# Kernel tuning notes

Measured on AMD Instinct MI355X. Metric: run time of the kernel, lower is better.

## Reference

```python
import jax, jax.numpy as jnp
import numpy as np

DIM = 64
WS = 8    # window_size
SS = 4    # shift_size


def _conv(x, w, pad, groups=1):
    return jax.lax.conv_general_dilated(
        x, w, (1, 1), ((pad, pad), (pad, pad)),
        dimension_numbers=('NCHW', 'OIHW', 'NCHW'),
        feature_group_count=groups)


def _window_partition(x, ws):
    # x: (B, C, H, W) -> (B*Hn*Wn, C, ws, ws), with bottom/right padding
    B, C, H, W = x.shape
    pb = (-H) % ws
    pr = (-W) % ws
    x = jnp.pad(x, ((0, 0), (0, 0), (0, pb), (0, pr)))
    Hp, Wp = H + pb, W + pr
    x = x.reshape(B, C, Hp // ws, ws, Wp // ws, ws).transpose(0, 1, 2, 4, 3, 5)
    return x.reshape(-1, C, ws, ws)


def _window_reverse(wins, ws, H, W):
    pb = (-H) % ws
    pr = (-W) % ws
    Hp, Wp = H + pb, W + pr
    B = wins.shape[0] // ((Hp // ws) * (Wp // ws))
    x = wins.reshape(B, -1, Hp // ws, Wp // ws, ws, ws).transpose(0, 1, 2, 4, 3, 5)
    x = x.reshape(B, -1, Hp, Wp)
    return x[:, :, :H, :W]


def _create_mask(H, W, ws, ss):
    # Swin-style additive mask, computed statically with numpy
    Hp = int(np.ceil(H / ws)) * ws
    Wp = int(np.ceil(W / ws)) * ws
    m = np.zeros((Hp, Wp), dtype=np.float32)
    slices = (slice(0, -ws), slice(-ws, -ss), slice(-ss, None))
    cnt = 0
    for hs in slices:
        for wsl in slices:
            m[hs, wsl] = cnt
            cnt += 1
    mw = m.reshape(Hp // ws, ws, Wp // ws, ws).transpose(0, 2, 1, 3).reshape(-1, ws * ws)
    diff = mw[:, None, :] - mw[:, :, None]
    return jnp.asarray(np.where(diff != 0, -100.0, 0.0).astype(np.float32))


def _l2norm(x):
    # matches torch F.normalize(dim=-1, eps=1e-12)
    return x / jnp.maximum(jnp.linalg.norm(x, axis=-1, keepdims=True), 1e-12)


def _win_attn(xw, w_qkv, w_dw, w_proj, ws, mask, b):
    # xw: (N, C, ws, ws) windows
    C = xw.shape[1]
    qkv = _conv(_conv(xw, w_qkv, 0), w_dw, 1, groups=3 * C)
    q, k, v = jnp.split(qkv, 3, axis=1)
    N = q.shape[0]
    hw = ws * ws
    q = _l2norm(q.reshape(N, C, hw))
    k = _l2norm(k.reshape(N, C, hw))
    v = v.reshape(N, C, hw)
    attn = jnp.einsum('nci,ncj->nij', q, k) / ws  # (N, hw, hw)
    if mask is not None:
        attn = (attn.reshape(b, -1, hw, hw) + mask[None]).reshape(-1, hw, hw)
    attn = jax.nn.softmax(attn, axis=-1)
    out = jnp.einsum('nci,nij->ncj', v, attn).reshape(N, C, ws, ws)
    return _conv(out, w_proj, 1)


def _forward(x, w_qkv0, w_dw0, w_proj0, w_qkv1, w_dw1, w_proj1):
    b, c, h, w = x.shape
    # pass 1: unshifted windows
    xw = _window_partition(x, WS)
    out = _win_attn(xw, w_qkv0, w_dw0, w_proj0, WS, None, b)
    out = _window_reverse(out, WS, h, w)
    # pass 2: shifted windows with Swin mask
    shift = jnp.roll(out, (-SS, -SS), axis=(2, 3))
    sw = _window_partition(shift, WS)
    mask = _create_mask(h, w, WS, SS)
    out = _win_attn(sw, w_qkv1, w_dw1, w_proj1, WS, mask, b)
    out = _window_reverse(out, WS, h, w)
    return jnp.roll(out, (SS, SS), axis=(2, 3))


def setup_inputs() -> dict:
    key = jax.random.key(0)
    ks = jax.random.split(key, 7)
    C = DIM
    s = 0.05
    return {
        'x': jax.random.normal(ks[0], (8, C, 256, 256), jnp.float32),
        'w_qkv0': jax.random.normal(ks[1], (3 * C, C, 1, 1), jnp.float32) * s,
        'w_dw0': jax.random.normal(ks[2], (3 * C, 1, 3, 3), jnp.float32) * s,
        'w_proj0': jax.random.normal(ks[3], (C, C, 3, 3), jnp.float32) * s,
        'w_qkv1': jax.random.normal(ks[4], (3 * C, C, 1, 1), jnp.float32) * s,
        'w_dw1': jax.random.normal(ks[5], (3 * C, 1, 3, 3), jnp.float32) * s,
        'w_proj1': jax.random.normal(ks[6], (C, C, 3, 3), jnp.float32) * s,
    }


def reference(x, w_qkv0, w_dw0, w_proj0, w_qkv1, w_dw1, w_proj1):
    return _forward(x, w_qkv0, w_dw0, w_proj0, w_qkv1, w_dw1, w_proj1)
```

## Files before the change

kernel.cpp:

```cpp
#include <hip/hip_runtime.h>


typedef __attribute__((ext_vector_type(8))) short bf8;
typedef __attribute__((ext_vector_type(4))) float f32x4;
#define MFMA(a, b, c) __builtin_amdgcn_mfma_f32_16x16x32_bf16(a, b, c, 0, 0, 0)

__device__ __forceinline__ int xkey(int p) { return ((p >> 3) ^ p) & 7; }
__device__ __forceinline__ int xswz(int p, int c) { return p * 64 + (c ^ (xkey(p) << 3)); }
__device__ __forceinline__ int pswz68(int ch, int p) {
    return ch * 68 + (p ^ (((ch >> 1) & 7) << 2));
}

__device__ __forceinline__ unsigned cvtpk(float a, float b) {
    unsigned r;
    asm("v_cvt_pk_bf16_f32 %0, %1, %2" : "=v"(r) : "v"(a), "v"(b));
    return r;
}

__device__ __forceinline__ void bsplit(float f, short& h, short& l) {
    unsigned u = __float_as_uint(f);
    unsigned hb = (u + 0x7FFFu + ((u >> 16) & 1u)) >> 16;
    float hf = __uint_as_float(hb << 16);
    float r = f - hf;
    unsigned u2 = __float_as_uint(r);
    unsigned lb = (u2 + 0x7FFFu + ((u2 >> 16) & 1u)) >> 16;
    h = (short)hb; l = (short)lb;
}
__device__ __forceinline__ void bsplit2(float a, float b, unsigned& hw, unsigned& lw) {
    hw = cvtpk(a, b);
    float ra = a - __uint_as_float(hw << 16);
    float rb = b - __uint_as_float(hw & 0xFFFF0000u);
    lw = cvtpk(ra, rb);
}

__global__ void k_fq(const float* __restrict__ wq, short* __restrict__ oh, short* __restrict__ ol) {
    int bx = blockIdx.x;
    int kk = bx / 12, tt = bx % 12;
    int tid = threadIdx.x;
    int lane = tid >> 3, j = tid & 7;
    int oc = tt * 16 + (lane & 15);
    int ic = kk * 32 + ((lane >> 4) << 3) + j;
    short h, l; bsplit(wq[oc * 64 + ic], h, l);
    oh[bx * 512 + tid] = h; ol[bx * 512 + tid] = l;
}
__global__ void k_fp(const float* __restrict__ wp, short* __restrict__ oh, short* __restrict__ ol) {
    int bx = blockIdx.x;
    int tap = bx >> 3, kk = (bx >> 2) & 1, tt = bx & 3;
    int tid = threadIdx.x;
    int lane = tid >> 3, j = tid & 7;
    int oc = tt * 16 + (lane & 15);
    int ic = kk * 32 + ((lane >> 4) << 3) + j;
    short h, l; bsplit(wp[(oc * 64 + ic) * 9 + tap], h, l);
    oh[bx * 512 + tid] = h; ol[bx * 512 + tid] = l;
}

__device__ __forceinline__ void dw_pair(const float* scr, const float* wd9,
                                        int ch0, int row, float o[2][8]) {
    #pragma unroll
    for (int chi = 0; chi < 2; ++chi) {
        int ch = ch0 + chi;
        const float* wd = wd9 + ch * 9;
        float w9[9];
        #pragma unroll
        for (int tp = 0; tp < 9; ++tp) w9[tp] = wd[tp];
        float e[3][10];
        #pragma unroll
        for (int k3 = 0; k3 < 3; ++k3) {
            int rr = row - 1 + k3;
            e[k3][0] = 0.f; e[k3][9] = 0.f;
            if ((unsigned)rr < 8u) {
                float4 a = *(const float4*)&scr[pswz68(ch, rr * 8)];
                float4 b = *(const float4*)&scr[pswz68(ch, rr * 8 + 4)];
                e[k3][1] = a.x; e[k3][2] = a.y; e[k3][3] = a.z; e[k3][4] = a.w;
                e[k3][5] = b.x; e[k3][6] = b.y; e[k3][7] = b.z; e[k3][8] = b.w;
            } else {
                #pragma unroll
                for (int q2 = 1; q2 < 9; ++q2) e[k3][q2] = 0.f;
            }
        }
        #pragma unroll
        for (int s = 0; s < 8; ++s) {
            float a = 0.f;
            #pragma unroll
            for (int k3 = 0; k3 < 3; ++k3)
                #pragma unroll
                for (int dx = 0; dx < 3; ++dx)
                    a = fmaf(w9[k3 * 3 + dx], e[k3][s + dx], a);
            o[chi][s] = a;
        }
    }
}

__device__ __forceinline__ void p2_chunk(const short* XTh, const short* XTl,
                                         const short* bqh, const short* bql,
                                         float* scr, int chunk,
                                         int mh, int nh, int col, int quad, int qo8, int lane)
{
    f32x4 acc[2][2];
    #pragma unroll
    for (int mt = 0; mt < 2; ++mt)
        #pragma unroll
        for (int nt = 0; nt < 2; ++nt) acc[mt][nt] = (f32x4){0.f, 0.f, 0.f, 0.f};
    #pragma unroll
    for (int kk = 0; kk < 2; ++kk) {
        bf8 Ah[2], Al[2];
        #pragma unroll
        for (int mt = 0; mt < 2; ++mt) {
            int row = (mh * 2 + mt) * 16 + col;
            int ad = row * 64 + ((kk * 32 + qo8) ^ (xkey(row) << 3));
            Ah[mt] = *(const bf8*)&XTh[ad];
            Al[mt] = *(const bf8*)&XTl[ad];
        }
        #pragma unroll
        for (int nt = 0; nt < 2; ++nt) {
            int tt = chunk * 4 + nh * 2 + nt;
            bf8 Bh = *(const bf8*)&bqh[((kk * 12 + tt) * 64 + lane) * 8];
            bf8 Bl = *(const bf8*)&bql[((kk * 12 + tt) * 64 + lane) * 8];
            #pragma unroll
            for (int mt = 0; mt < 2; ++mt) {
                acc[mt][nt] = MFMA(Ah[mt], Bh, acc[mt][nt]);
                acc[mt][nt] = MFMA(Ah[mt], Bl, acc[mt][nt]);
                acc[mt][nt] = MFMA(Al[mt], Bh, acc[mt][nt]);
            }
        }
    }
    #pragma unroll
    for (int nt = 0; nt < 2; ++nt) {
        int oc = (nh * 2 + nt) * 16 + col;
        #pragma unroll
        for (int mt = 0; mt < 2; ++mt) {
            int p0 = (mh * 2 + mt) * 16 + quad * 4;
            *(f32x4*)&scr[pswz68(oc, p0)] = acc[mt][nt];
        }
    }
}

__global__ __launch_bounds__(256, 3)
void k_fused(const float* __restrict__ in,
             const short* __restrict__ bqh, const short* __restrict__ bql,
             const float* __restrict__ wdw,
             const short* __restrict__ bph, const short* __restrict__ bpl,
             float* __restrict__ out, int shift, int use_mask, int roll)
{
    __shared__ __align__(16) char smem[50432];
    short* XTh = (short*)smem;
    short* XTl = (short*)(smem + 8320);
    float* scr = (float*)(smem + 16640);
    short* vbh = (short*)(smem + 16640);
    short* vbl = (short*)(smem + 24832);
    float* projo = (float*)(smem + 16640);
    short* kTh = (short*)(smem + 34048);
    short* kTl = (short*)(smem + 42240);
    short* PTh = kTh;
    short* PTl = kTl;

    const int tid = threadIdx.x, lane = tid & 63, wv = tid >> 6;
    const int col = lane & 15, quad = lane >> 4, qo8 = quad * 8;
    const int mh = wv & 1, nh = wv >> 1;
    const int cp = tid >> 3, rrow = tid & 7;
    const int n = blockIdx.x;
    const int b = n >> 10, c = (n >> 4) & 63, t = n & 15;
    const size_t base = ((size_t)(b * 64 + c)) << 16;

    #pragma unroll
    for (int k = 0; k < 16; k += 2) {
        int o0 = tid + k * 256, o1 = o0 + 256;
        int hi0 = o0 >> 11, r0 = (o0 >> 8) & 7, lo0 = (o0 >> 3) & 31, s0 = o0 & 7;
        int hi1 = o1 >> 11, r1 = (o1 >> 8) & 7, lo1 = (o1 >> 3) & 31, s1 = o1 & 7;
        float v0 = in[base + (size_t)(((t * 16 + hi0 * 8 + r0) + shift) & 255) * 256
                           + (((lo0 * 8 + s0) + shift) & 255)];
        float v1 = in[base + (size_t)(((t * 16 + hi1 * 8 + r1) + shift) & 255) * 256
                           + (((lo1 * 8 + s1) + shift) & 255)];
        unsigned hw, lw; bsplit2(v0, v1, hw, lw);
        int ad0 = xswz(r0 * 8 + s0, hi0 * 32 + lo0);
        int ad1 = xswz(r1 * 8 + s1, hi1 * 32 + lo1);
        XTh[ad0] = (short)hw; XTh[ad1] = (short)(hw >> 16);
        XTl[ad0] = (short)lw; XTl[ad1] = (short)(lw >> 16);
    }
    __syncthreads();

    p2_chunk(XTh, XTl, bqh, bql, scr, 0, mh, nh, col, quad, qo8, lane);
    __syncthreads();

    float dq[2][8], nq[2];
    dw_pair(scr, wdw, 2 * cp, rrow, dq);
    #pragma unroll
    for (int chi = 0; chi < 2; ++chi) {
        float ss = 0.f;
        #pragma unroll
        for (int s = 0; s < 8; ++s) ss = fmaf(dq[chi][s], dq[chi][s], ss);
        ss += __shfl_xor(ss, 1); ss += __shfl_xor(ss, 2); ss += __shfl_xor(ss, 4);
        nq[chi] = fmaxf(sqrtf(ss), 1e-12f);
    }
    __syncthreads();

    p2_chunk(XTh, XTl, bqh, bql, scr, 1, mh, nh, col, quad, qo8, lane);
    __syncthreads();

    {
        float dk[2][8];
        dw_pair(scr, wdw + 64 * 9, 2 * cp, rrow, dk);
        #pragma unroll
        for (int chi = 0; chi < 2; ++chi) {
            float ss = 0.f;
            #pragma unroll
            for (int s = 0; s < 8; ++s) ss = fmaf(dk[chi][s], dk[chi][s], ss);
            ss += __shfl_xor(ss, 1); ss += __shfl_xor(ss, 2); ss += __shfl_xor(ss, 4);
            float nk = fmaxf(sqrtf(ss), 1e-12f);
            float sc = 0.125f / (nq[chi] * nk);
            #pragma unroll
            for (int s = 0; s < 8; ++s) dk[chi][s] *= sc;
        }
        #pragma unroll
        for (int s0 = 0; s0 < 8; ++s0) {
            unsigned hw, lw; bsplit2(dk[0][s0], dk[1][s0], hw, lw);
            int ad = xswz(rrow * 8 + s0, 2 * cp);
            *(unsigned*)&kTh[ad] = hw; *(unsigned*)&kTl[ad] = lw;
        }
    }
    __syncthreads();

    p2_chunk(XTh, XTl, bqh, bql, scr, 2, mh, nh, col, quad, qo8, lane);
    __syncthreads();

    float dv[2][8];
    dw_pair(scr, wdw + 128 * 9, 2 * cp, rrow, dv);
    #pragma unroll
    for (int s0 = 0; s0 < 8; ++s0) {
        unsigned hw, lw; bsplit2(dq[0][s0], dq[1][s0], hw, lw);
        int ad = xswz(rrow * 8 + s0, 2 * cp);
        *(unsigned*)&XTh[ad] = hw; *(unsigned*)&XTl[ad] = lw;
    }
    if (tid < 32) {
        *(unsigned*)&XTh[4096 + 2 * tid] = 0u;
        *(unsigned*)&XTl[4096 + 2 * tid] = 0u;
    }
    __syncthreads();

    #pragma unroll
    for (int chi = 0; chi < 2; ++chi) {
        unsigned hw[4], lw[4];
        #pragma unroll
        for (int q2 = 0; q2 < 4; ++q2) bsplit2(dv[chi][2 * q2], dv[chi][2 * q2 + 1], hw[q2], lw[q2]);
        int ch = 2 * cp + chi;
        int ad = ch * 64 + ((rrow ^ xkey(ch)) << 3);
        *(uint4*)&vbh[ad] = (uint4){hw[0], hw[1], hw[2], hw[3]};
        *(uint4*)&vbl[ad] = (uint4){lw[0], lw[1], lw[2], lw[3]};
    }

    f32x4 at[4];
    #pragma unroll
    for (int nt = 0; nt < 4; ++nt) at[nt] = (f32x4){0.f, 0.f, 0.f, 0.f};
    {
        bf8 Ah[2], Al[2];
        #pragma unroll
        for (int kk = 0; kk < 2; ++kk) {
            int row = wv * 16 + col;
            int ad = row * 64 + ((kk * 32 + qo8) ^ (xkey(row) << 3));
            Ah[kk] = *(const bf8*)&XTh[ad];
            Al[kk] = *(const bf8*)&XTl[ad];
        }
        #pragma unroll
        for (int kk = 0; kk < 2; ++kk)
            #pragma unroll
            for (int nt = 0; nt < 4; ++nt) {
                int rowB = nt * 16 + col;
                int ad = rowB * 64 + ((kk * 32 + qo8) ^ (xkey(rowB) << 3));
                bf8 Bh = *(const bf8*)&kTh[ad];
                bf8 Bl = *(const bf8*)&kTl[ad];
                at[nt] = MFMA(Ah[kk], Bh, at[nt]);
                at[nt] = MFMA(Ah[kk], Bl, at[nt]);
                at[nt] = MFMA(Al[kk], Bh, at[nt]);
            }
    }
    if (use_mask) {
        const int widx = n & 1023;
        const int hn_m = widx >> 5, wn_m = widx & 31;
        #pragma unroll
        for (int nt = 0; nt < 4; ++nt) {
            int j = nt * 16 + col;
            int rj = ((hn_m == 31) ? (((j >> 3) < 4) ? 1 : 2) : 0) * 3
                   + ((wn_m == 31) ? (((j & 7) < 4) ? 1 : 2) : 0);
            #pragma unroll
            for (int rg = 0; rg < 4; ++rg) {
                int i = wv * 16 + quad * 4 + rg;
                int ri = ((hn_m == 31) ? (((i >> 3) < 4) ? 1 : 2) : 0) * 3
                       + ((wn_m == 31) ? (((i & 7) < 4) ? 1 : 2) : 0);
                if (ri != rj) at[nt][rg] = at[nt][rg] - 100.f;
            }
        }
    }
    float Pv[4][4];
    #pragma unroll
    for (int rg = 0; rg < 4; ++rg) {
        float m = fmaxf(fmaxf(at[0][rg], at[1][rg]), fmaxf(at[2][rg], at[3][rg]));
        m = fmaxf(m, __shfl_xor(m, 1)); m = fmaxf(m, __shfl_xor(m, 2));
        m = fmaxf(m, __shfl_xor(m, 4)); m = fmaxf(m, __shfl_xor(m, 8));
        float e0 = __expf(at[0][rg] - m), e1 = __expf(at[1][rg] - m);
        float e2 = __expf(at[2][rg] - m), e3 = __expf(at[3][rg] - m);
        float s = e0 + e1 + e2 + e3;
        s += __shfl_xor(s, 1); s += __shfl_xor(s, 2);
        s += __shfl_xor(s, 4); s += __shfl_xor(s, 8);
        float is = 1.0f / s;
        Pv[0][rg] = e0 * is; Pv[1][rg] = e1 * is; Pv[2][rg] = e2 * is; Pv[3][rg] = e3 * is;
    }
    __syncthreads();

    #pragma unroll
    for (int nt = 0; nt < 4; ++nt) {
        int j = nt * 16 + col;
        #pragma unroll
        for (int rp = 0; rp < 2; ++rp) {
            unsigned hw, lw; bsplit2(Pv[nt][2 * rp], Pv[nt][2 * rp + 1], hw, lw);
            int i0 = wv * 16 + quad * 4 + 2 * rp;
            int ad = j * 64 + (i0 ^ (xkey(j) << 3));
            *(unsigned*)&PTh[ad] = hw; *(unsigned*)&PTl[ad] = lw;
        }
    }
    __syncthreads();

    {
        f32x4 av[2][2];
        #pragma unroll
        for (int mt = 0; mt < 2; ++mt)
            #pragma unroll
            for (int nt = 0; nt < 2; ++nt) av[mt][nt] = (f32x4){0.f, 0.f, 0.f, 0.f};
        #pragma unroll
        for (int kk = 0; kk < 2; ++kk) {
            bf8 Ah[2], Al[2], Bh[2], Bl[2];
            #pragma unroll
            for (int mt = 0; mt < 2; ++mt) {
                int row = (mh * 2 + mt) * 16 + col;
                int ad = row * 64 + ((kk * 32 + qo8) ^ (xkey(row) << 3));
                Ah[mt] = *(const bf8*)&vbh[ad];
                Al[mt] = *(const bf8*)&vbl[ad];
            }
            #pragma unroll
            for (int nt = 0; nt < 2; ++nt) {
                int rowB = (nh * 2 + nt) * 16 + col;
                int ad = rowB * 64 + ((kk * 32 + qo8) ^ (xkey(rowB) << 3));
                Bh[nt] = *(const bf8*)&PTh[ad];
                Bl[nt] = *(const bf8*)&PTl[ad];
            }
            #pragma unroll
            for (int mt = 0; mt < 2; ++mt)
                #pragma unroll
                for (int nt = 0; nt < 2; ++nt) {
                    av[mt][nt] = MFMA(Ah[mt], Bh[nt], av[mt][nt]);
                    av[mt][nt] = MFMA(Ah[mt], Bl[nt], av[mt][nt]);
                    av[mt][nt] = MFMA(Al[mt], Bh[nt], av[mt][nt]);
                }
        }
        #pragma unroll
        for (int nt = 0; nt < 2; ++nt) {
            int j = (nh * 2 + nt) * 16 + col;
            #pragma unroll
            for (int mt = 0; mt < 2; ++mt) {
                int c0 = (mh * 2 + mt) * 16 + quad * 4;
                #pragma unroll
                for (int rp = 0; rp < 2; ++rp) {
                    unsigned hw, lw; bsplit2(av[mt][nt][2 * rp], av[mt][nt][2 * rp + 1], hw, lw);
                    int ad = j * 64 + ((c0 + 2 * rp) ^ (xkey(j) << 3));
                    *(unsigned*)&XTh[ad] = hw;
                    *(unsigned*)&XTl[ad] = lw;
                }
            }
        }
    }
    __syncthreads();

    {
        f32x4 ap[2][2];
        #pragma unroll
        for (int mt = 0; mt < 2; ++mt)
            #pragma unroll
            for (int nt = 0; nt < 2; ++nt) ap[mt][nt] = (f32x4){0.f, 0.f, 0.f, 0.f};
        const int smc = col & 7;
        #pragma unroll 1
        for (int tap = 0; tap < 9; ++tap) {
            int dy = (tap >= 6) ? 1 : ((tap >= 3) ? 0 : -1);
            int dx = tap - (dy + 1) * 3 - 1;
            int ra[2];
            #pragma unroll
            for (int mt = 0; mt < 2; ++mt) {
                int rr = (mh * 2 + mt) * 2 + (col >> 3) + dy;
                int ss = smc + dx;
                bool ok = ((unsigned)rr < 8u) && ((unsigned)ss < 8u);
                ra[mt] = ok ? (rr * 8 + ss) : 64;
            }
            #pragma unroll
            for (int kk = 0; kk < 2; ++kk) {
                bf8 Bh[2], Bl[2], Ah[2], Al[2];
                #pragma unroll
                for (int nt = 0; nt < 2; ++nt) {
                    int bi = (((tap * 2 + kk) * 4 + (nh * 2 + nt)) * 64 + lane) * 8;
                    Bh[nt] = *(const bf8*)&bph[bi];
                    Bl[nt] = *(const bf8*)&bpl[bi];
                }
                #pragma unroll
                for (int mt = 0; mt < 2; ++mt) {
                    int ad = ra[mt] * 64 + ((kk * 32 + qo8) ^ (xkey(ra[mt]) << 3));
                    Ah[mt] = *(const bf8*)&XTh[ad];
                    Al[mt] = *(const bf8*)&XTl[ad];
                }
                #pragma unroll
                for (int mt = 0; mt < 2; ++mt)
                    #pragma unroll
                    for (int nt = 0; nt < 2; ++nt) {
                        ap[mt][nt] = MFMA(Ah[mt], Bh[nt], ap[mt][nt]);
                        ap[mt][nt] = MFMA(Ah[mt], Bl[nt], ap[mt][nt]);
                        ap[mt][nt] = MFMA(Al[mt], Bh[nt], ap[mt][nt]);
                    }
            }
        }
        #pragma unroll
        for (int nt = 0; nt < 2; ++nt) {
            int oc = (nh * 2 + nt) * 16 + col;
            #pragma unroll
            for (int mt = 0; mt < 2; ++mt) {
                int p0 = (mh * 2 + mt) * 16 + quad * 4;
                *(f32x4*)&projo[pswz68(oc, p0)] = ap[mt][nt];
            }
        }
    }
    __syncthreads();

    #pragma unroll
    for (int k = 0; k < 16; ++k) {
        int o = tid + k * 256;
        int hi = o >> 11, r = (o >> 8) & 7, lo = (o >> 3) & 31, s = o & 7;
        int c2 = hi * 32 + lo;
        float v = projo[pswz68(c2, r * 8 + s)];
        int h2 = t * 16 + hi * 8 + r, w2 = lo * 8 + s;
        out[base + (size_t)((h2 + roll) & 255) * 256 + ((w2 + roll) & 255)] = v;
    }
}

extern "C" void kernel_launch(void* const* d_in, const int* in_sizes, int n_in,
                              void* d_out, int out_size, void* d_ws, size_t ws_size,
                              hipStream_t stream)
{
    const float* x      = (const float*)d_in[0];
    const float* wqkv0  = (const float*)d_in[1];
    const float* wdw0   = (const float*)d_in[2];
    const float* wproj0 = (const float*)d_in[3];
    const float* wqkv1  = (const float*)d_in[4];
    const float* wdw1   = (const float*)d_in[5];
    const float* wproj1 = (const float*)d_in[6];
    float* out = (float*)d_out;

    float* tmp = (float*)d_ws;
    short* fb  = (short*)(tmp + 33554432);
    short* bq0h = fb;
    short* bq0l = fb + 12288;
    short* bq1h = fb + 24576;
    short* bq1l = fb + 36864;
    short* bp0h = fb + 49152;
    short* bp0l = fb + 86016;
    short* bp1h = fb + 122880;
    short* bp1l = fb + 159744;

    hipLaunchKernelGGL(k_fq, dim3(24), dim3(512), 0, stream, wqkv0, bq0h, bq0l);
    hipLaunchKernelGGL(k_fq, dim3(24), dim3(512), 0, stream, wqkv1, bq1h, bq1l);
    hipLaunchKernelGGL(k_fp, dim3(72), dim3(512), 0, stream, wproj0, bp0h, bp0l);
    hipLaunchKernelGGL(k_fp, dim3(72), dim3(512), 0, stream, wproj1, bp1h, bp1l);

    hipLaunchKernelGGL(k_fused, dim3(8192), dim3(256), 0, stream,
                       x, bq0h, bq0l, wdw0, bp0h, bp0l, tmp, 0, 0, 0);
    hipLaunchKernelGGL(k_fused, dim3(8192), dim3(256), 0, stream,
                       tmp, bq1h, bq1l, wdw1, bp1h, bp1l, out, 4, 1, 4);
}
```

Baseline: 635.6 us.

## Shrink shared memory to fit four blocks per CU by chunking QKV and PV stages

Cuts the fused window-attention kernel's LDS footprint from about 50KB to 40KB and raises the launch bound from 3 to 4 blocks per CU. The QKV projection is now computed in six 32-channel chunks instead of three 64-channel ones, and each thread handles one channel instead of two in the depthwise conv. The P·V stage is split into two halves that reuse a smaller P buffer. Buffers are aliased more aggressively, and the zero-padding row for the projection conv moves to a separate location. The aim is higher occupancy, paid for with more __syncthreads barriers and smaller MFMA tiles per wave.

```diff
diff --git a/kernel.cpp b/kernel.cpp
--- a/kernel.cpp
+++ b/kernel.cpp
@@ -7,8 +7,11 @@
 
 __device__ __forceinline__ int xkey(int p) { return ((p >> 3) ^ p) & 7; }
 __device__ __forceinline__ int xswz(int p, int c) { return p * 64 + (c ^ (xkey(p) << 3)); }
-__device__ __forceinline__ int pswz68(int ch, int p) {
-    return ch * 68 + (p ^ (((ch >> 1) & 7) << 2));
+__device__ __forceinline__ int sswz(int ch, int p) {
+    return ch * 64 + (p ^ (((ch >> 1) & 7) << 2));
+}
+__device__ __forceinline__ int jswz(int ch, int p) {
+    return ch * 64 + (p ^ (((ch >> 1) & 7) << 3));
 }
 
 __device__ __forceinline__ unsigned cvtpk(float a, float b) {
@@ -54,53 +57,54 @@
     oh[bx * 512 + tid] = h; ol[bx * 512 + tid] = l;
 }
 
-__device__ __forceinline__ void dw_pair(const float* scr, const float* wd9,
-                                        int ch0, int row, float o[2][8]) {
-    #pragma unroll
-    for (int chi = 0; chi < 2; ++chi) {
-        int ch = ch0 + chi;
-        const float* wd = wd9 + ch * 9;
-        float w9[9];
-        #pragma unroll
-        for (int tp = 0; tp < 9; ++tp) w9[tp] = wd[tp];
-        float e[3][10];
-        #pragma unroll
-        for (int k3 = 0; k3 < 3; ++k3) {
-            int rr = row - 1 + k3;
-            e[k3][0] = 0.f; e[k3][9] = 0.f;
-            if ((unsigned)rr < 8u) {
-                float4 a = *(const float4*)&scr[pswz68(ch, rr * 8)];
-                float4 b = *(const float4*)&scr[pswz68(ch, rr * 8 + 4)];
-                e[k3][1] = a.x; e[k3][2] = a.y; e[k3][3] = a.z; e[k3][4] = a.w;
-                e[k3][5] = b.x; e[k3][6] = b.y; e[k3][7] = b.z; e[k3][8] = b.w;
-            } else {
-                #pragma unroll
-                for (int q2 = 1; q2 < 9; ++q2) e[k3][q2] = 0.f;
-            }
-        }
-        #pragma unroll
-        for (int s = 0; s < 8; ++s) {
-            float a = 0.f;
-            #pragma unroll
-            for (int k3 = 0; k3 < 3; ++k3)
-                #pragma unroll
-                for (int dx = 0; dx < 3; ++dx)
-                    a = fmaf(w9[k3 * 3 + dx], e[k3][s + dx], a);
-            o[chi][s] = a;
-        }
-    }
-}
-
-__device__ __forceinline__ void p2_chunk(const short* XTh, const short* XTl,
-                                         const short* bqh, const short* bql,
-                                         float* scr, int chunk,
-                                         int mh, int nh, int col, int quad, int qo8, int lane)
+__device__ __forceinline__ void dw_one(const float* scr, const float* wd,
+                                       int ch, int row, float o[8]) {
+    float w9[9];
+    #pragma unroll
+    for (int tp = 0; tp < 9; ++tp) w9[tp] = wd[tp];
+    float e[3][10];
+    #pragma unroll
+    for (int k3 = 0; k3 < 3; ++k3) {
+        int rr = row - 1 + k3;
+        e[k3][0] = 0.f; e[k3][9] = 0.f;
+        if ((unsigned)rr < 8u) {
+            float4 a = *(const float4*)&scr[sswz(ch, rr * 8)];
+            float4 b = *(const float4*)&scr[sswz(ch, rr * 8 + 4)];
+            e[k3][1] = a.x; e[k3][2] = a.y; e[k3][3] = a.z; e[k3][4] = a.w;
+            e[k3][5] = b.x; e[k3][6] = b.y; e[k3][7] = b.z; e[k3][8] = b.w;
+        } else {
+            #pragma unroll
+            for (int q2 = 1; q2 < 9; ++q2) e[k3][q2] = 0.f;
+        }
+    }
+    #pragma unroll
+    for (int s = 0; s < 8; ++s) {
+        float a = 0.f;
+        #pragma unroll
+        for (int k3 = 0; k3 < 3; ++k3)
+            #pragma unroll
+            for (int dx = 0; dx < 3; ++dx)
+                a = fmaf(w9[k3 * 3 + dx], e[k3][s + dx], a);
+        o[s] = a;
+    }
+}
+
+__device__ __forceinline__ float norm8(const float d[8]) {
+    float ss = 0.f;
+    #pragma unroll
+    for (int s = 0; s < 8; ++s) ss = fmaf(d[s], d[s], ss);
+    ss += __shfl_xor(ss, 1); ss += __shfl_xor(ss, 2); ss += __shfl_xor(ss, 4);
+    return fmaxf(sqrtf(ss), 1e-12f);
+}
+
+__device__ __forceinline__ void p2_chunk32(const short* XTh, const short* XTl,
+                                           const short* bqh, const short* bql,
+                                           float* scr, int chunk,
+                                           int mh, int nh, int col, int quad, int qo8, int lane)
 {
-    f32x4 acc[2][2];
-    #pragma unroll
-    for (int mt = 0; mt < 2; ++mt)
-        #pragma unroll
-        for (int nt = 0; nt < 2; ++nt) acc[mt][nt] = (f32x4){0.f, 0.f, 0.f, 0.f};
+    f32x4 acc[2];
+    #pragma unroll
+    for (int mt = 0; mt < 2; ++mt) acc[mt] = (f32x4){0.f, 0.f, 0.f, 0.f};
     #pragma unroll
     for (int kk = 0; kk < 2; ++kk) {
         bf8 Ah[2], Al[2];
@@ -111,53 +115,47 @@
             Ah[mt] = *(const bf8*)&XTh[ad];
             Al[mt] = *(const bf8*)&XTl[ad];
         }
-        #pragma unroll
-        for (int nt = 0; nt < 2; ++nt) {
-            int tt = chunk * 4 + nh * 2 + nt;
-            bf8 Bh = *(const bf8*)&bqh[((kk * 12 + tt) * 64 + lane) * 8];
-            bf8 Bl = *(const bf8*)&bql[((kk * 12 + tt) * 64 + lane) * 8];
-            #pragma unroll
-            for (int mt = 0; mt < 2; ++mt) {
-                acc[mt][nt] = MFMA(Ah[mt], Bh, acc[mt][nt]);
-                acc[mt][nt] = MFMA(Ah[mt], Bl, acc[mt][nt]);
-                acc[mt][nt] = MFMA(Al[mt], Bh, acc[mt][nt]);
-            }
-        }
-    }
-    #pragma unroll
-    for (int nt = 0; nt < 2; ++nt) {
-        int oc = (nh * 2 + nt) * 16 + col;
+        int tt = chunk * 2 + nh;
+        bf8 Bh = *(const bf8*)&bqh[((kk * 12 + tt) * 64 + lane) * 8];
+        bf8 Bl = *(const bf8*)&bql[((kk * 12 + tt) * 64 + lane) * 8];
         #pragma unroll
         for (int mt = 0; mt < 2; ++mt) {
-            int p0 = (mh * 2 + mt) * 16 + quad * 4;
-            *(f32x4*)&scr[pswz68(oc, p0)] = acc[mt][nt];
-        }
-    }
-}
-
-__global__ __launch_bounds__(256, 3)
+            acc[mt] = MFMA(Ah[mt], Bh, acc[mt]);
+            acc[mt] = MFMA(Ah[mt], Bl, acc[mt]);
+            acc[mt] = MFMA(Al[mt], Bh, acc[mt]);
+        }
+    }
+    #pragma unroll
+    for (int mt = 0; mt < 2; ++mt) {
+        int ocl = nh * 16 + col;
+        int p0 = (mh * 2 + mt) * 16 + quad * 4;
+        *(f32x4*)&scr[sswz(ocl, p0)] = acc[mt];
+    }
+}
+
+__global__ __launch_bounds__(256, 4)
 void k_fused(const float* __restrict__ in,
              const short* __restrict__ bqh, const short* __restrict__ bql,
              const float* __restrict__ wdw,
              const short* __restrict__ bph, const short* __restrict__ bpl,
              float* __restrict__ out, int shift, int use_mask, int roll)
 {
-    __shared__ __align__(16) char smem[50432];
+    __shared__ __align__(16) char smem[40960];
     short* XTh = (short*)smem;
-    short* XTl = (short*)(smem + 8320);
-    float* scr = (float*)(smem + 16640);
-    short* vbh = (short*)(smem + 16640);
-    short* vbl = (short*)(smem + 24832);
-    float* projo = (float*)(smem + 16640);
-    short* kTh = (short*)(smem + 34048);
-    short* kTl = (short*)(smem + 42240);
-    short* PTh = kTh;
-    short* PTl = kTl;
+    short* XTl = (short*)(smem + 8192);
+    short* kTh = (short*)(smem + 16384);
+    short* kTl = (short*)(smem + 24576);
+    short* vbh = kTh;
+    short* vbl = kTl;
+    float* scr = (float*)(smem + 32768);
+    short* PTh = (short*)(smem + 32768);
+    short* PTl = (short*)(smem + 36864);
+    float* projo = (float*)(smem + 16384);
 
     const int tid = threadIdx.x, lane = tid & 63, wv = tid >> 6;
     const int col = lane & 15, quad = lane >> 4, qo8 = quad * 8;
     const int mh = wv & 1, nh = wv >> 1;
-    const int cp = tid >> 3, rrow = tid & 7;
+    const int ch = tid >> 3, rrow = tid & 7;
     const int n = blockIdx.x;
     const int b = n >> 10, c = (n >> 4) & 63, t = n & 15;
     const size_t base = ((size_t)(b * 64 + c)) << 16;
@@ -179,74 +177,83 @@
     }
     __syncthreads();
 
-    p2_chunk(XTh, XTl, bqh, bql, scr, 0, mh, nh, col, quad, qo8, lane);
-    __syncthreads();
-
-    float dq[2][8], nq[2];
-    dw_pair(scr, wdw, 2 * cp, rrow, dq);
-    #pragma unroll
-    for (int chi = 0; chi < 2; ++chi) {
-        float ss = 0.f;
-        #pragma unroll
-        for (int s = 0; s < 8; ++s) ss = fmaf(dq[chi][s], dq[chi][s], ss);
-        ss += __shfl_xor(ss, 1); ss += __shfl_xor(ss, 2); ss += __shfl_xor(ss, 4);
-        nq[chi] = fmaxf(sqrtf(ss), 1e-12f);
-    }
-    __syncthreads();
-
-    p2_chunk(XTh, XTl, bqh, bql, scr, 1, mh, nh, col, quad, qo8, lane);
-    __syncthreads();
-
+    float dqA[8], dqB[8], dvA[8], dvB[8];
+    float nqA, nqB;
+
+    p2_chunk32(XTh, XTl, bqh, bql, scr, 0, mh, nh, col, quad, qo8, lane);
+    __syncthreads();
+    dw_one(scr, wdw + ch * 9, ch, rrow, dqA);
+    nqA = norm8(dqA);
+    __syncthreads();
+    p2_chunk32(XTh, XTl, bqh, bql, scr, 1, mh, nh, col, quad, qo8, lane);
+    __syncthreads();
+    dw_one(scr, wdw + (32 + ch) * 9, ch, rrow, dqB);
+    nqB = norm8(dqB);
+    __syncthreads();
+    p2_chunk32(XTh, XTl, bqh, bql, scr, 2, mh, nh, col, quad, qo8, lane);
+    __syncthreads();
     {
-        float dk[2][8];
-        dw_pair(scr, wdw + 64 * 9, 2 * cp, rrow, dk);
-        #pragma unroll
-        for (int chi = 0; chi < 2; ++chi) {
-            float ss = 0.f;
-            #pragma unroll
-            for (int s = 0; s < 8; ++s) ss = fmaf(dk[chi][s], dk[chi][s], ss);
-            ss += __shfl_xor(ss, 1); ss += __shfl_xor(ss, 2); ss += __shfl_xor(ss, 4);
-            float nk = fmaxf(sqrtf(ss), 1e-12f);
-            float sc = 0.125f / (nq[chi] * nk);
-            #pragma unroll
-            for (int s = 0; s < 8; ++s) dk[chi][s] *= sc;
-        }
-        #pragma unroll
-        for (int s0 = 0; s0 < 8; ++s0) {
-            unsigned hw, lw; bsplit2(dk[0][s0], dk[1][s0], hw, lw);
-            int ad = xswz(rrow * 8 + s0, 2 * cp);
-            *(unsigned*)&kTh[ad] = hw; *(unsigned*)&kTl[ad] = lw;
-        }
-    }
-    __syncthreads();
-
-    p2_chunk(XTh, XTl, bqh, bql, scr, 2, mh, nh, col, quad, qo8, lane);
-    __syncthreads();
-
-    float dv[2][8];
-    dw_pair(scr, wdw + 128 * 9, 2 * cp, rrow, dv);
-    #pragma unroll
-    for (int s0 = 0; s0 < 8; ++s0) {
-        unsigned hw, lw; bsplit2(dq[0][s0], dq[1][s0], hw, lw);
-        int ad = xswz(rrow * 8 + s0, 2 * cp);
-        *(unsigned*)&XTh[ad] = hw; *(unsigned*)&XTl[ad] = lw;
-    }
-    if (tid < 32) {
-        *(unsigned*)&XTh[4096 + 2 * tid] = 0u;
-        *(unsigned*)&XTl[4096 + 2 * tid] = 0u;
-    }
-    __syncthreads();
-
-    #pragma unroll
-    for (int chi = 0; chi < 2; ++chi) {
-        unsigned hw[4], lw[4];
-        #pragma unroll
-        for (int q2 = 0; q2 < 4; ++q2) bsplit2(dv[chi][2 * q2], dv[chi][2 * q2 + 1], hw[q2], lw[q2]);
-        int ch = 2 * cp + chi;
-        int ad = ch * 64 + ((rrow ^ xkey(ch)) << 3);
-        *(uint4*)&vbh[ad] = (uint4){hw[0], hw[1], hw[2], hw[3]};
-        *(uint4*)&vbl[ad] = (uint4){lw[0], lw[1], lw[2], lw[3]};
-    }
+        float dk[8];
+        dw_one(scr, wdw + (64 + ch) * 9, ch, rrow, dk);
+        float sc = 0.125f / (nqA * norm8(dk));
+        #pragma unroll
+        for (int s = 0; s < 8; ++s) dk[s] *= sc;
+        #pragma unroll
+        for (int s0 = 0; s0 < 8; s0 += 2) {
+            unsigned hw, lw; bsplit2(dk[s0], dk[s0 + 1], hw, lw);
+            int p0 = rrow * 8 + s0;
+            int a0 = xswz(p0, ch), a1 = xswz(p0 + 1, ch);
+            kTh[a0] = (short)hw; kTh[a1] = (short)(hw >> 16);
+            kTl[a0] = (short)lw; kTl[a1] = (short)(lw >> 16);
+        }
+    }
+    __syncthreads();
+    p2_chunk32(XTh, XTl, bqh, bql, scr, 3, mh, nh, col, quad, qo8, lane);
+    __syncthreads();
+    {
+        float dk[8];
+        dw_one(scr, wdw + (96 + ch) * 9, ch, rrow, dk);
+        float sc = 0.125f / (nqB * norm8(dk));
+        #pragma unroll
+        for (int s = 0; s < 8; ++s) dk[s] *= sc;
+        int cg = 32 + ch;
+        #pragma unroll
+        for (int s0 = 0; s0 < 8; s0 += 2) {
+            unsigned hw, lw; bsplit2(dk[s0], dk[s0 + 1], hw, lw);
+            int p0 = rrow * 8 + s0;
+            int a0 = xswz(p0, cg), a1 = xswz(p0 + 1, cg);
+            kTh[a0] = (short)hw; kTh[a1] = (short)(hw >> 16);
+            kTl[a0] = (short)lw; kTl[a1] = (short)(lw >> 16);
+        }
+    }
+    __syncthreads();
+    p2_chunk32(XTh, XTl, bqh, bql, scr, 4, mh, nh, col, quad, qo8, lane);
+    __syncthreads();
+    dw_one(scr, wdw + (128 + ch) * 9, ch, rrow, dvA);
+    __syncthreads();
+    p2_chunk32(XTh, XTl, bqh, bql, scr, 5, mh, nh, col, quad, qo8, lane);
+    __syncthreads();
+    dw_one(scr, wdw + (160 + ch) * 9, ch, rrow, dvB);
+    #pragma unroll
+    for (int s0 = 0; s0 < 8; s0 += 2) {
+        unsigned hw, lw; bsplit2(dqA[s0], dqA[s0 + 1], hw, lw);
+        int p0 = rrow * 8 + s0;
+        int a0 = xswz(p0, ch), a1 = xswz(p0 + 1, ch);
+        XTh[a0] = (short)hw; XTh[a1] = (short)(hw >> 16);
+        XTl[a0] = (short)lw; XTl[a1] = (short)(lw >> 16);
+    }
+    {
+        int cg = 32 + ch;
+        #pragma unroll
+        for (int s0 = 0; s0 < 8; s0 += 2) {
+            unsigned hw, lw; bsplit2(dqB[s0], dqB[s0 + 1], hw, lw);
+            int p0 = rrow * 8 + s0;
+            int a0 = xswz(p0, cg), a1 = xswz(p0 + 1, cg);
+            XTh[a0] = (short)hw; XTh[a1] = (short)(hw >> 16);
+            XTl[a0] = (short)lw; XTl[a1] = (short)(lw >> 16);
+        }
+    }
+    __syncthreads();
 
     f32x4 at[4];
     #pragma unroll
@@ -307,27 +314,53 @@
     __syncthreads();
 
     #pragma unroll
-    for (int nt = 0; nt < 4; ++nt) {
-        int j = nt * 16 + col;
+    for (int hf = 0; hf < 2; ++hf) {
+        const float* dv = hf ? dvB : dvA;
+        int cg = hf * 32 + ch;
+        unsigned hw[4], lw[4];
+        #pragma unroll
+        for (int q2 = 0; q2 < 4; ++q2) bsplit2(dv[2 * q2], dv[2 * q2 + 1], hw[q2], lw[q2]);
+        int ad = cg * 64 + ((rrow ^ xkey(cg)) << 3);
+        *(uint4*)&vbh[ad] = (uint4){hw[0], hw[1], hw[2], hw[3]};
+        *(uint4*)&vbl[ad] = (uint4){lw[0], lw[1], lw[2], lw[3]};
+    }
+    #pragma unroll
+    for (int q = 0; q < 2; ++q) {
+        int nt = q;
+        int jl = q * 16 + col;
         #pragma unroll
         for (int rp = 0; rp < 2; ++rp) {
             unsigned hw, lw; bsplit2(Pv[nt][2 * rp], Pv[nt][2 * rp + 1], hw, lw);
             int i0 = wv * 16 + quad * 4 + 2 * rp;
-            int ad = j * 64 + (i0 ^ (xkey(j) << 3));
+            int ad = jl * 64 + (i0 ^ (xkey(jl) << 3));
             *(unsigned*)&PTh[ad] = hw; *(unsigned*)&PTl[ad] = lw;
         }
     }
     __syncthreads();
 
-    {
-        f32x4 av[2][2];
-        #pragma unroll
-        for (int mt = 0; mt < 2; ++mt)
-            #pragma unroll
-            for (int nt = 0; nt < 2; ++nt) av[mt][nt] = (f32x4){0.f, 0.f, 0.f, 0.f};
+    #pragma unroll
+    for (int h = 0; h < 2; ++h) {
+        if (h == 1) {
+            #pragma unroll
+            for (int q = 0; q < 2; ++q) {
+                int nt = 2 + q;
+                int jl = q * 16 + col;
+                #pragma unroll
+                for (int rp = 0; rp < 2; ++rp) {
+                    unsigned hw, lw; bsplit2(Pv[nt][2 * rp], Pv[nt][2 * rp + 1], hw, lw);
+                    int i0 = wv * 16 + quad * 4 + 2 * rp;
+                    int ad = jl * 64 + (i0 ^ (xkey(jl) << 3));
+                    *(unsigned*)&PTh[ad] = hw; *(unsigned*)&PTl[ad] = lw;
+                }
+            }
+            __syncthreads();
+        }
+        f32x4 av[2];
+        #pragma unroll
+        for (int mt = 0; mt < 2; ++mt) av[mt] = (f32x4){0.f, 0.f, 0.f, 0.f};
         #pragma unroll
         for (int kk = 0; kk < 2; ++kk) {
-            bf8 Ah[2], Al[2], Bh[2], Bl[2];
+            bf8 Ah[2], Al[2];
             #pragma unroll
             for (int mt = 0; mt < 2; ++mt) {
                 int row = (mh * 2 + mt) * 16 + col;
@@ -335,38 +368,33 @@
                 Ah[mt] = *(const bf8*)&vbh[ad];
                 Al[mt] = *(const bf8*)&vbl[ad];
             }
-            #pragma unroll
-            for (int nt = 0; nt < 2; ++nt) {
-                int rowB = (nh * 2 + nt) * 16 + col;
-                int ad = rowB * 64 + ((kk * 32 + qo8) ^ (xkey(rowB) << 3));
-                Bh[nt] = *(const bf8*)&PTh[ad];
-                Bl[nt] = *(const bf8*)&PTl[ad];
-            }
-            #pragma unroll
-            for (int mt = 0; mt < 2; ++mt)
-                #pragma unroll
-                for (int nt = 0; nt < 2; ++nt) {
-                    av[mt][nt] = MFMA(Ah[mt], Bh[nt], av[mt][nt]);
-                    av[mt][nt] = MFMA(Ah[mt], Bl[nt], av[mt][nt]);
-                    av[mt][nt] = MFMA(Al[mt], Bh[nt], av[mt][nt]);
-                }
-        }
-        #pragma unroll
-        for (int nt = 0; nt < 2; ++nt) {
-            int j = (nh * 2 + nt) * 16 + col;
+            int jl = nh * 16 + col;
+            int bd = jl * 64 + ((kk * 32 + qo8) ^ (xkey(jl) << 3));
+            bf8 Bh = *(const bf8*)&PTh[bd];
+            bf8 Bl = *(const bf8*)&PTl[bd];
             #pragma unroll
             for (int mt = 0; mt < 2; ++mt) {
-                int c0 = (mh * 2 + mt) * 16 + quad * 4;
-                #pragma unroll
-                for (int rp = 0; rp < 2; ++rp) {
-                    unsigned hw, lw; bsplit2(av[mt][nt][2 * rp], av[mt][nt][2 * rp + 1], hw, lw);
-                    int ad = j * 64 + ((c0 + 2 * rp) ^ (xkey(j) << 3));
-                    *(unsigned*)&XTh[ad] = hw;
-                    *(unsigned*)&XTl[ad] = lw;
-                }
-            }
-        }
-    }
+                av[mt] = MFMA(Ah[mt], Bh, av[mt]);
+                av[mt] = MFMA(Ah[mt], Bl, av[mt]);
+                av[mt] = MFMA(Al[mt], Bh, av[mt]);
+            }
+        }
+        int j = (h * 2 + nh) * 16 + col;
+        #pragma unroll
+        for (int mt = 0; mt < 2; ++mt) {
+            int c0 = (mh * 2 + mt) * 16 + quad * 4;
+            #pragma unroll
+            for (int rp = 0; rp < 2; ++rp) {
+                unsigned hw, lw; bsplit2(av[mt][2 * rp], av[mt][2 * rp + 1], hw, lw);
+                int ad = j * 64 + ((c0 + 2 * rp) ^ (xkey(j) << 3));
+                *(unsigned*)&XTh[ad] = hw;
+                *(unsigned*)&XTl[ad] = lw;
+            }
+        }
+        __syncthreads();
+    }
+
+    if (tid < 32) ((unsigned*)(smem + 32768))[tid] = 0u;
     __syncthreads();
 
     {
@@ -380,13 +408,15 @@
         for (int tap = 0; tap < 9; ++tap) {
             int dy = (tap >= 6) ? 1 : ((tap >= 3) ? 0 : -1);
             int dx = tap - (dy + 1) * 3 - 1;
-            int ra[2];
+            int ra_h[2], ra_l[2];
             #pragma unroll
             for (int mt = 0; mt < 2; ++mt) {
                 int rr = (mh * 2 + mt) * 2 + (col >> 3) + dy;
                 int ss = smc + dx;
                 bool ok = ((unsigned)rr < 8u) && ((unsigned)ss < 8u);
-                ra[mt] = ok ? (rr * 8 + ss) : 64;
+                int row = rr * 8 + ss;
+                ra_h[mt] = ok ? row : 256;
+                ra_l[mt] = ok ? row : 192;
             }
             #pragma unroll
             for (int kk = 0; kk < 2; ++kk) {
@@ -399,9 +429,10 @@
                 }
                 #pragma unroll
                 for (int mt = 0; mt < 2; ++mt) {
-                    int ad = ra[mt] * 64 + ((kk * 32 + qo8) ^ (xkey(ra[mt]) << 3));
-                    Ah[mt] = *(const bf8*)&XTh[ad];
-                    Al[mt] = *(const bf8*)&XTl[ad];
+                    int adh = ra_h[mt] * 64 + ((kk * 32 + qo8) ^ (xkey(ra_h[mt]) << 3));
+                    int adl = ra_l[mt] * 64 + ((kk * 32 + qo8) ^ (xkey(ra_l[mt]) << 3));
+                    Ah[mt] = *(const bf8*)&XTh[adh];
+                    Al[mt] = *(const bf8*)&XTl[adl];
                 }
                 #pragma unroll
                 for (int mt = 0; mt < 2; ++mt)
@@ -419,7 +450,7 @@
             #pragma unroll
             for (int mt = 0; mt < 2; ++mt) {
                 int p0 = (mh * 2 + mt) * 16 + quad * 4;
-                *(f32x4*)&projo[pswz68(oc, p0)] = ap[mt][nt];
+                *(f32x4*)&projo[jswz(oc, p0)] = ap[mt][nt];
             }
         }
     }
@@ -430,7 +461,7 @@
         int o = tid + k * 256;
         int hi = o >> 11, r = (o >> 8) & 7, lo = (o >> 3) & 31, s = o & 7;
         int c2 = hi * 32 + lo;
-        float v = projo[pswz68(c2, r * 8 + s)];
+        float v = projo[jswz(c2, r * 8 + s)];
         int h2 = t * 16 + hi * 8 + r, w2 = lo * 8 + s;
         out[base + (size_t)((h2 + roll) & 255) * 256 + ((w2 + roll) & 255)] = v;
     }
```

Measured after the change: 624.2 us. Within noise of the previous version (-1.8%).
